# Optimization experiments

Hardware: AMD Instinct MI355X
Metric: run time of the kernel (lower is better)

The kernel has to match this reference:

```python
import jax, jax.numpy as jnp
import numpy as np

B, L, N, T, D, V, C = 128, 512, 1023, 511, 256, 50000, 511
EPS = 1e-6


def circular_correlation(a, b):
    # c_k = sum_i a_i * b_{(i+k) mod d}  == irfft(conj(rfft(a)) * rfft(b))
    d = a.shape[-1]
    c = jnp.fft.irfft(jnp.conj(jnp.fft.rfft(a, axis=-1)) * jnp.fft.rfft(b, axis=-1), n=d, axis=-1)
    return c / (jnp.linalg.norm(c, axis=-1, keepdims=True) + EPS)


def setup_inputs() -> dict:
    key = jax.random.key(0)
    k1, k2, k3, k4, k5, k6, k7, k8 = jax.random.split(key, 8)
    num_node = jnp.full((B,), N, dtype=jnp.int64 if jax.config.jax_enable_x64 else jnp.int32)
    # leaf slot index: leaves occupy node slots 0..L-1 (deterministic, no scatter collisions)
    slot = jnp.broadcast_to(jnp.arange(L, dtype=jnp.int32)[None, :], (B, L))
    vocab_id = jax.random.randint(k1, (B, L), 0, V, dtype=jnp.int32)
    leaf_content_id = jnp.stack([slot, vocab_id], axis=-1)  # [B, L, 2]
    content_mask = (jax.random.uniform(k2, (B, L)) < 0.9).astype(jnp.int32)
    ctype = jax.random.randint(k3, (B, T), 0, 3, dtype=jnp.int32)          # 0 = no-op, 1, 2 children
    parent = jax.random.randint(k4, (B, T), L, N, dtype=jnp.int32)         # internal node slots
    lchild = jax.random.randint(k5, (B, T), 0, N, dtype=jnp.int32)
    rchild = jax.random.randint(k6, (B, T), 0, N, dtype=jnp.int32)
    composition_info = jnp.stack([ctype, parent, lchild, rchild], axis=-1)  # [B, T, 4]
    emb_weight = jax.random.normal(k7, (V, D), dtype=jnp.float32) * 0.1
    lin_weight = jax.random.normal(k8, (C, D), dtype=jnp.float32) * 0.05
    lin_bias = jnp.zeros((C,), dtype=jnp.float32)
    return {"num_node": num_node, "leaf_content_id": leaf_content_id,
            "content_mask": content_mask, "composition_info": composition_info,
            "emb_weight": emb_weight, "lin_weight": lin_weight, "lin_bias": lin_bias}


def embed_leaf_nodes(leaf_content_id, content_mask, emb_weight):
    leaf_vec = emb_weight[leaf_content_id[:, :, 1]]          # [B, L, D]
    node_idx = leaf_content_id[:, :, 0]                      # [B, L]
    mask = content_mask != 0
    safe_idx = jnp.where(mask, node_idx, N)                  # N is out-of-bounds -> dropped
    vec = jnp.zeros((B, N, D), dtype=leaf_vec.dtype)
    vec = vec.at[jnp.arange(B)[:, None], safe_idx].set(leaf_vec, mode="drop")
    norm = jnp.linalg.norm(vec, axis=2, keepdims=True) + EPS
    return vec / norm


def compose(vec, composition_info):
    bidx = jnp.arange(B)

    def step(v, info):  # info: [B, 4] for one tree level
        t, p, l, r = info[:, 0], info[:, 1], info[:, 2], info[:, 3]
        safe_p = jnp.where(t > 0, p, 0)
        lv = v[bidx, l]                                      # [B, D]
        rv = v[bidx, r]
        two = circular_correlation(lv, rv)
        cur = v[bidx, safe_p]
        val = jnp.where((t == 1)[:, None], lv,
                        jnp.where((t == 2)[:, None], two, cur))
        return v.at[bidx, safe_p].set(val), None

    vec, _ = jax.lax.scan(step, vec, jnp.swapaxes(composition_info, 0, 1))
    return vec


def reference(num_node, leaf_content_id, content_mask, composition_info,
              emb_weight, lin_weight, lin_bias):
    vec = embed_leaf_nodes(leaf_content_id, content_mask, emb_weight)
    vec = compose(vec, composition_info)
    out = jnp.einsum("bnd,cd->bnc", vec, lin_weight) + lin_bias
    return out
```

## Files before the change

kernel.cpp:

```cpp
#include <hip/hip_runtime.h>

#define NB 128
#define NL 512
#define NN 1023
#define NT 511
#define ND 256
#define NC 511
#define EPSF 1e-6f

#define SRC_ZERO (-1)
#define SLOTC 4096
#define STEPC 8192

typedef __attribute__((ext_vector_type(8))) short short8;
typedef __attribute__((ext_vector_type(4))) float f32x4;
typedef __attribute__((ext_vector_type(2))) float f32x2;

__device__ __forceinline__ unsigned short f2bf(float f) {
  unsigned u = __builtin_bit_cast(unsigned, f);
  u += 0x7FFFu + ((u >> 16) & 1u);
  return (unsigned short)(u >> 16);
}

__global__ void __launch_bounds__(256) embed_scatter(
    const int* __restrict__ lcid, const int* __restrict__ cmask,
    const float* __restrict__ emb, const float* __restrict__ lw,
    float* __restrict__ leafbuf, unsigned short* __restrict__ vecb,
    unsigned short* __restrict__ wb) {
  if (blockIdx.x >= 16384) {
    int i   = (blockIdx.x - 16384) * 256 + threadIdx.x;
    int row = i >> 5;
    uint4 r = {0u, 0u, 0u, 0u};
    if (row < NC) {
      const float4* v4 = (const float4*)lw;
      float4 x = v4[2 * i], y = v4[2 * i + 1];
      r.x = (unsigned)f2bf(x.x) | ((unsigned)f2bf(x.y) << 16);
      r.y = (unsigned)f2bf(x.z) | ((unsigned)f2bf(x.w) << 16);
      r.z = (unsigned)f2bf(y.x) | ((unsigned)f2bf(y.y) << 16);
      r.w = (unsigned)f2bf(y.z) | ((unsigned)f2bf(y.w) << 16);
    }
    ((uint4*)wb)[i] = r;
    return;
  }
  int rid  = blockIdx.x * 4 + (threadIdx.x >> 6);
  int lane = threadIdx.x & 63;
  int slot = lcid[2 * rid];
  int vid  = lcid[2 * rid + 1];
  int msk  = cmask[rid];
  int b    = rid >> 9;
  float4 v = {0.f, 0.f, 0.f, 0.f};
  if (msk) v = ((const float4*)(emb + (size_t)vid * ND))[lane];
  float ss = v.x * v.x + v.y * v.y + v.z * v.z + v.w * v.w;
#pragma unroll
  for (int off = 32; off > 0; off >>= 1) ss += __shfl_down(ss, off, 64);
  ss = __shfl(ss, 0, 64);
  float inv = 1.0f / (sqrtf(ss) + EPSF);
  float4 o;
  o.x = v.x * inv; o.y = v.y * inv; o.z = v.z * inv; o.w = v.w * inv;
  ((float4*)(leafbuf + ((size_t)b * 512 + slot) * ND))[lane] = o;
  uint2 pk;
  pk.x = (unsigned)f2bf(o.x) | ((unsigned)f2bf(o.y) << 16);
  pk.y = (unsigned)f2bf(o.z) | ((unsigned)f2bf(o.w) << 16);
  ((uint2*)(vecb + ((size_t)b * NN + slot) * ND))[lane] = pk;
}

struct ComposeSh {
  int4 sinfo4[NT];
  int ptr_[NT];
  int lsA[NT], rsA[NT];
  int lvl[NT], fsrc[NT];
  int schedS[NT], schedL[NT], schedR[NT];
  int offs[512], cnt[512], cnt2[512];
  unsigned char deadF[NT], liveF[NT], lzero[512];
  float a_st[16][256];
  float b_st[16][512];
  float s_st[16][512];
  int changed, smax;
};
struct LeafGemmSh { short As[256 * 64]; short Ws[128 * 64]; };
union FuseSh { ComposeSh c; LeafGemmSh g; };

__global__ void __launch_bounds__(1024) compose_leafgemm(
    const int* __restrict__ info, const int* __restrict__ lcid,
    const int* __restrict__ cmask, const float* __restrict__ leafbuf,
    float* __restrict__ outbuf, int* __restrict__ fsrcG,
    const short* __restrict__ vecbS, const short* __restrict__ wbs,
    const float* __restrict__ bias, float* __restrict__ out) {
  __shared__ FuseSh sh;
  const int tid  = threadIdx.x;
  const int lane = tid & 63;
  const int wav  = tid >> 6;

  if (blockIdx.x < NB) {
    const int b = blockIdx.x;
    int4 (&sinfo4)[NT] = sh.c.sinfo4;
    int (&ptr_)[NT] = sh.c.ptr_;
    int (&lsA)[NT] = sh.c.lsA;  int (&rsA)[NT] = sh.c.rsA;
    int (&lvl)[NT] = sh.c.lvl;  int (&fsrc)[NT] = sh.c.fsrc;
    int (&schedS)[NT] = sh.c.schedS; int (&schedL)[NT] = sh.c.schedL;
    int (&schedR)[NT] = sh.c.schedR;
    int (&offs)[512] = sh.c.offs; int (&cnt)[512] = sh.c.cnt;
    int (&cnt2)[512] = sh.c.cnt2;
    unsigned char (&deadF)[NT] = sh.c.deadF;
    unsigned char (&liveF)[NT] = sh.c.liveF;
    unsigned char (&lzero)[512] = sh.c.lzero;
    float (&a_st)[16][256] = sh.c.a_st;
    float (&b_st)[16][512] = sh.c.b_st;
    float (&s_st)[16][512] = sh.c.s_st;
    int &changed = sh.c.changed; int &smax = sh.c.smax;

    const float* lb = leafbuf + (size_t)b * 512 * ND;
    float*       ob = outbuf + (size_t)b * NT * ND;

    const int4* ib4 = (const int4*)(info + (size_t)b * NT * 4);
    for (int i = tid; i < NT; i += 1024) sinfo4[i] = ib4[i];
    if (tid < 512) lzero[tid] = 1;
    if (tid == 0) smax = 0;
    __syncthreads();
    if (tid < NL) {
      int row = lcid[((size_t)b * NL + tid) * 2];
      lzero[row] = (cmask[(size_t)b * NL + tid] == 0) ? 1 : 0;
    }
    __syncthreads();

    const int t = tid;
    int4 m1 = {0, 0, 0, 0};
    if (t < NT) m1 = sinfo4[t];
    int l1 = -1, r1 = -1, f1 = -1;
    const int prow = 512 + t;
    for (int tp = 0; tp < NT; ++tp) {
      int4 wi = sinfo4[tp];
      if (wi.x > 0) {
        if (t < NT && tp < t) { if (wi.y == m1.z) l1 = tp; if (wi.y == m1.w) r1 = tp; }
        if (wi.y == prow) f1 = tp;
      }
    }
    __syncthreads();

    if (t < NT) {
      int v;
      if (m1.x == 2) v = SLOTC + t;
      else if (m1.x == 1) {
        if (m1.z < 512) v = m1.z;
        else v = (l1 >= 0) ? (STEPC + l1) : SRC_ZERO;
      } else v = SRC_ZERO;
      ptr_[t] = v;
    }
    __syncthreads();
    for (int it = 0; it < 10; ++it) {
      int v = 0;
      if (t < NT) { v = ptr_[t]; if (v >= STEPC) v = ptr_[v - STEPC]; }
      __syncthreads();
      if (t < NT) ptr_[t] = v;
      __syncthreads();
    }

    auto normv = [&](int v) -> int {
      if (v >= 0 && v < 512 && lzero[v]) return SRC_ZERO;
      return v;
    };
    auto collapseW = [&](int wstep) -> int {
      int v = (sinfo4[wstep].x == 2) ? (SLOTC + wstep) : ptr_[wstep];
      return normv(v);
    };
    if (t < NT) {
      if (m1.x == 2) {
        int a = (m1.z < 512) ? normv(m1.z) : ((l1 >= 0) ? collapseW(l1) : SRC_ZERO);
        int c = (m1.w < 512) ? normv(m1.w) : ((r1 >= 0) ? collapseW(r1) : SRC_ZERO);
        lsA[t] = a; rsA[t] = c;
        deadF[t] = (a == SRC_ZERO || c == SRC_ZERO) ? 1 : 0;
      } else {
        deadF[t] = 0;
      }
      liveF[t] = 0;
      fsrc[t] = (f1 >= 0) ? collapseW(f1) : SRC_ZERO;
    }
    __syncthreads();

    for (int rounds = 0; rounds < NT; ++rounds) {
      if (tid == 0) changed = 0;
      __syncthreads();
      if (t < NT && m1.x == 2 && !deadF[t]) {
        int a = lsA[t], c = rsA[t];
        if (a >= SLOTC && deadF[a - SLOTC]) { a = SRC_ZERO; lsA[t] = a; }
        if (c >= SLOTC && deadF[c - SLOTC]) { c = SRC_ZERO; rsA[t] = c; }
        if (a == SRC_ZERO || c == SRC_ZERO) { deadF[t] = 1; changed = 1; }
      }
      __syncthreads();
      if (!changed) break;
      __syncthreads();
    }

    if (t < NT) {
      int f = fsrc[t];
      if (f >= SLOTC && deadF[f - SLOTC]) { f = SRC_ZERO; fsrc[t] = f; }
      if (f >= SLOTC) liveF[f - SLOTC] = 1;
    }
    __syncthreads();
    for (int rounds = 0; rounds < NT; ++rounds) {
      if (tid == 0) changed = 0;
      __syncthreads();
      if (t < NT && m1.x == 2 && liveF[t] && !deadF[t]) {
        int a = lsA[t], c = rsA[t];
        if (a >= SLOTC && !liveF[a - SLOTC]) { liveF[a - SLOTC] = 1; changed = 1; }
        if (c >= SLOTC && !liveF[c - SLOTC]) { liveF[c - SLOTC] = 1; changed = 1; }
      }
      __syncthreads();
      if (!changed) break;
      __syncthreads();
    }

    const bool isLive = (t < NT && m1.x == 2 && liveF[t] && !deadF[t]);

    if (t < NT) lvl[t] = 0;
    __syncthreads();
    for (int rounds = 0; rounds < NT; ++rounds) {
      if (tid == 0) changed = 0;
      __syncthreads();
      if (isLive) {
        int nl = 1, a = lsA[t], c = rsA[t];
        if (a >= SLOTC) { int dl = lvl[a - SLOTC] + 1; if (dl > nl) nl = dl; }
        if (c >= SLOTC) { int dl = lvl[c - SLOTC] + 1; if (dl > nl) nl = dl; }
        if (nl > lvl[t]) { lvl[t] = nl; changed = 1; }
      }
      __syncthreads();
      if (!changed) break;
      __syncthreads();
    }
    if (isLive) atomicMax(&smax, lvl[t]);

    if (tid < 512) { cnt[tid] = 0; cnt2[tid] = 0; }
    __syncthreads();
    if (isLive) atomicAdd(&cnt[lvl[t]], 1);
    __syncthreads();
    if (tid < 512) offs[tid] = cnt[tid];
    __syncthreads();
    for (int k = 1; k < 512; k <<= 1) {
      int v = 0;
      if (tid < 512) { v = offs[tid]; if (tid >= k) v += offs[tid - k]; }
      __syncthreads();
      if (tid < 512) offs[tid] = v;
      __syncthreads();
    }
    if (isLive) {
      int d = lvl[t];
      int pos = offs[d - 1] + atomicAdd(&cnt2[d], 1);
      schedS[pos] = t; schedL[pos] = lsA[t]; schedR[pos] = rsA[t];
    }
    __syncthreads();

    const int maxd = smax;
    for (int d = 1; d <= maxd; ++d) {
      const int base = offs[d - 1];
      const int nops = cnt[d];
      const int nch  = (nops + 15) >> 4;
      for (int ch = 0; ch < nch; ++ch) {
        int rel = ch * 16 + wav;
        if (rel < nops) {
          int my = base + rel;
          int tt = schedS[my], ls = schedL[my], rs = schedR[my];
          const float* pa = (ls < 512) ? lb + (size_t)ls * ND
                                       : ob + (size_t)(ls - SLOTC) * ND;
          const float* pb = (rs < 512) ? lb + (size_t)rs * ND
                                       : ob + (size_t)(rs - SLOTC) * ND;
          float4 av = ((const float4*)pa)[lane];
          float4 bv = ((const float4*)pb)[lane];
          float nx = __shfl(bv.x, (lane + 1) & 63, 64);
          float4 sv = {bv.y, bv.z, bv.w, nx};
          ((float4*)a_st[wav])[lane]      = av;
          ((float4*)b_st[wav])[lane]      = bv;
          ((float4*)b_st[wav])[lane + 64] = bv;
          ((float4*)s_st[wav])[lane]      = sv;
          ((float4*)s_st[wav])[lane + 64] = sv;
          const float4* a4 = (const float4*)a_st[wav];
          const float4* b4 = (const float4*)b_st[wav];
          const float4* s4 = (const float4*)s_st[wav];
          f32x2 q0 = {0.f, 0.f}, q1 = {0.f, 0.f}, q2 = {0.f, 0.f}, q3 = {0.f, 0.f};
          float4 B0 = b4[lane];
          float4 S0 = s4[lane];
#pragma unroll 8
          for (int i = 0; i < 64; ++i) {
            float4 A  = a4[i];
            float4 B1 = b4[lane + i + 1];
            float4 S1 = s4[lane + i + 1];
            f32x2 Axy = {A.x, A.y},  Azw = {A.z, A.w};
            f32x2 Bxy = {B0.x, B0.y}, Bzw = {B0.z, B0.w};
            f32x2 Sxy = {S0.x, S0.y}, Szw = {S0.z, S0.w};
            f32x2 B1xy = {B1.x, B1.y}, S1xy = {S1.x, S1.y};
            q0 += Axy * Bxy;  q0 += Azw * Bzw;
            q1 += Axy * Sxy;  q1 += Azw * Szw;
            q2 += Axy * Bzw;  q2 += Azw * B1xy;
            q3 += Axy * Szw;  q3 += Azw * S1xy;
            B0 = B1; S0 = S1;
          }
          float c0 = q0.x + q0.y, c1 = q1.x + q1.y;
          float c2 = q2.x + q2.y, c3 = q3.x + q3.y;
          float ss = c0 * c0 + c1 * c1 + c2 * c2 + c3 * c3;
#pragma unroll
          for (int off = 32; off > 0; off >>= 1) ss += __shfl_down(ss, off, 64);
          ss = __shfl(ss, 0, 64);
          float inv = 1.f / (sqrtf(ss) + EPSF);
          float4 res;
          res.x = c0 * inv; res.y = c1 * inv; res.z = c2 * inv; res.w = c3 * inv;
          ((float4*)(ob + (size_t)tt * ND))[lane] = res;
        }
      }
      __syncthreads();
    }

    for (int i = tid; i < NT; i += 1024) fsrcG[b * NT + i] = fsrc[i];
    return;
  }

  const int gidx = blockIdx.x - NB;
  const int b  = gidx >> 3;
  const int mt = (gidx >> 2) & 1;
  const int ct = gidx & 3;
  const short* A = vecbS + ((size_t)b * NN + mt * 256) * ND;
  const int c0   = ct * 128;
  const int wr   = wav >> 1;
  const int wc   = wav & 1;
  const int frow = lane & 15;
  const int quad = lane >> 4;
  f32x4 acc[2][4];
#pragma unroll
  for (int i = 0; i < 2; ++i)
#pragma unroll
    for (int j = 0; j < 4; ++j) acc[i][j] = (f32x4){0.f, 0.f, 0.f, 0.f};

  for (int k0 = 0; k0 < ND; k0 += 64) {
#pragma unroll
    for (int i = 0; i < 2; ++i) {
      int idx = i * 1024 + tid;
      int row = idx >> 3;
      int chn = idx & 7;
      const short* ga = A + (size_t)row * ND + k0 + chn * 8;
      __builtin_amdgcn_global_load_lds(
          (const __attribute__((address_space(1))) void*)ga,
          (__attribute__((address_space(3))) void*)(sh.g.As + idx * 8), 16, 0, 0);
    }
    {
      int row = tid >> 3;
      int chn = tid & 7;
      const short* gw = wbs + (size_t)(c0 + row) * ND + k0 + chn * 8;
      __builtin_amdgcn_global_load_lds(
          (const __attribute__((address_space(1))) void*)gw,
          (__attribute__((address_space(3))) void*)(sh.g.Ws + tid * 8), 16, 0, 0);
    }
    __syncthreads();
#pragma unroll
    for (int ks = 0; ks < 2; ++ks) {
      short8 af[2], wf[4];
#pragma unroll
      for (int mi = 0; mi < 2; ++mi)
        af[mi] = *(const short8*)(sh.g.As + (wr * 32 + mi * 16 + frow) * 64 + ks * 32 + quad * 8);
#pragma unroll
      for (int ci = 0; ci < 4; ++ci)
        wf[ci] = *(const short8*)(sh.g.Ws + (wc * 64 + ci * 16 + frow) * 64 + ks * 32 + quad * 8);
#pragma unroll
      for (int mi = 0; mi < 2; ++mi)
#pragma unroll
        for (int ci = 0; ci < 4; ++ci)
          acc[mi][ci] = __builtin_amdgcn_mfma_f32_16x16x32_bf16(
              af[mi], wf[ci], acc[mi][ci], 0, 0, 0);
    }
    __syncthreads();
  }
#pragma unroll
  for (int mi = 0; mi < 2; ++mi) {
#pragma unroll
    for (int ci = 0; ci < 4; ++ci) {
      int col = c0 + wc * 64 + ci * 16 + frow;
      if (col < NC) {
        float bv = bias[col];
#pragma unroll
        for (int r = 0; r < 4; ++r) {
          int n = mt * 256 + wr * 32 + mi * 16 + quad * 4 + r;
          out[((size_t)b * NN + n) * NC + col] = acc[mi][ci][r] + bv;
        }
      }
    }
  }
}

__global__ void __launch_bounds__(256) gather_rows(
    const int* __restrict__ fsrcG, const float* __restrict__ leafbuf,
    const float* __restrict__ outbuf, unsigned short* __restrict__ vecb) {
  int rid  = blockIdx.x * 4 + (threadIdx.x >> 6);
  int lane = threadIdx.x & 63;
  int b    = rid / NT;
  int idx  = rid - b * NT;
  int s    = fsrcG[rid];
  float4 v = {0.f, 0.f, 0.f, 0.f};
  if (s >= 0) {
    const float* src = (s < 512)
        ? (leafbuf + ((size_t)b * 512 + s) * ND)
        : (outbuf + ((size_t)b * NT + (s - SLOTC)) * ND);
    v = ((const float4*)src)[lane];
  }
  uint2 pk;
  pk.x = (unsigned)f2bf(v.x) | ((unsigned)f2bf(v.y) << 16);
  pk.y = (unsigned)f2bf(v.z) | ((unsigned)f2bf(v.w) << 16);
  ((uint2*)(vecb + ((size_t)b * NN + 512 + idx) * ND))[lane] = pk;
}

union GemmSh {
  struct { short As[128 * 64]; short Ws[128 * 64]; } s;
  float epi[4][16][65];
};

__global__ void __launch_bounds__(256) gemm_int(
    const short* __restrict__ A, const short* __restrict__ W,
    const float* __restrict__ bias, float* __restrict__ out) {
  __shared__ GemmSh sh;
  int i = blockIdx.x;
  int mtile = (i >> 5) * 8 + (i & 7);
  int c     = (i >> 3) & 3;
  int b     = mtile >> 2;
  int mt    = mtile & 3;
  size_t arow = (size_t)b * NN + 512 + mt * 128;
  int tid  = threadIdx.x;
  int lane = tid & 63;
  int w    = tid >> 6;
  int c0   = c * 128;
  int wm   = (w & 1) * 64;
  int wc   = (w >> 1) * 64;
  int frow = lane & 15;
  int quad = lane >> 4;
  f32x4 acc[4][4];
#pragma unroll
  for (int a = 0; a < 4; ++a)
#pragma unroll
    for (int j = 0; j < 4; ++j) acc[a][j] = (f32x4){0.f, 0.f, 0.f, 0.f};

  for (int k0 = 0; k0 < ND; k0 += 64) {
#pragma unroll
    for (int a = 0; a < 4; ++a) {
      int idx = a * 256 + tid;
      int row = idx >> 3;
      int ch  = idx & 7;
      int chs = ch ^ (row & 7);
      const short* ga = A + (arow + row) * ND + k0 + chs * 8;
      const short* gw = W + (size_t)(c0 + row) * ND + k0 + chs * 8;
      __builtin_amdgcn_global_load_lds(
          (const __attribute__((address_space(1))) void*)ga,
          (__attribute__((address_space(3))) void*)(sh.s.As + idx * 8), 16, 0, 0);
      __builtin_amdgcn_global_load_lds(
          (const __attribute__((address_space(1))) void*)gw,
          (__attribute__((address_space(3))) void*)(sh.s.Ws + idx * 8), 16, 0, 0);
    }
    __syncthreads();
#pragma unroll
    for (int ks = 0; ks < 2; ++ks) {
      short8 af[4], wf[4];
#pragma unroll
      for (int mi = 0; mi < 4; ++mi) {
        int r = wm + mi * 16 + frow;
        int cc = (ks * 4 + quad) ^ (r & 7);
        af[mi] = *(const short8*)(sh.s.As + r * 64 + cc * 8);
      }
#pragma unroll
      for (int ci = 0; ci < 4; ++ci) {
        int r = wc + ci * 16 + frow;
        int cc = (ks * 4 + quad) ^ (r & 7);
        wf[ci] = *(const short8*)(sh.s.Ws + r * 64 + cc * 8);
      }
#pragma unroll
      for (int mi = 0; mi < 4; ++mi)
#pragma unroll
        for (int ci = 0; ci < 4; ++ci)
          acc[mi][ci] = __builtin_amdgcn_mfma_f32_16x16x32_bf16(
              af[mi], wf[ci], acc[mi][ci], 0, 0, 0);
    }
    __syncthreads();
  }

  int colg = c0 + wc + lane;
  float bv = (colg < NC) ? bias[colg] : 0.f;
#pragma unroll
  for (int mi = 0; mi < 4; ++mi) {
#pragma unroll
    for (int ci = 0; ci < 4; ++ci)
#pragma unroll
      for (int r = 0; r < 4; ++r)
        sh.epi[w][quad * 4 + r][ci * 16 + frow] = acc[mi][ci][r];
    if (colg < NC) {
      int nbase = 512 + mt * 128 + wm + mi * 16;
#pragma unroll
      for (int rr = 0; rr < 16; ++rr) {
        int n = nbase + rr;
        if (n < NN)
          out[((size_t)b * NN + n) * NC + colg] = sh.epi[w][rr][lane] + bv;
      }
    }
  }
}

extern "C" void kernel_launch(void* const* d_in, const int* in_sizes, int n_in,
                              void* d_out, int out_size, void* d_ws, size_t ws_size,
                              hipStream_t stream) {
  const int*   lcid  = (const int*)d_in[1];
  const int*   cmask = (const int*)d_in[2];
  const int*   cinfo = (const int*)d_in[3];
  const float* emb   = (const float*)d_in[4];
  const float* lw    = (const float*)d_in[5];
  const float* lbias = (const float*)d_in[6];
  float*       out   = (float*)d_out;

  char* ws = (char*)d_ws;
  float*          leafbuf = (float*)ws;
  float*          outbuf  = (float*)(ws + 67108864);
  unsigned short* vecb    = (unsigned short*)(ws + 134086656);
  unsigned short* wb      = (unsigned short*)(ws + 201129984);
  int*            fsrcG   = (int*)d_out + (size_t)512 * NC;

  embed_scatter<<<16448, 256, 0, stream>>>(lcid, cmask, emb, lw,
                                           leafbuf, vecb, wb);
  compose_leafgemm<<<NB + 1024, 1024, 0, stream>>>(
      cinfo, lcid, cmask, leafbuf, outbuf, fsrcG,
      (const short*)vecb, (const short*)wb, lbias, out);
  gather_rows<<<NB * NT / 4, 256, 0, stream>>>(fsrcG, leafbuf, outbuf, vecb);
  gemm_int<<<2048, 256, 0, stream>>>(
      (const short*)vecb, (const short*)wb, lbias, out);
}
```

Baseline: 480.5 us.

## Fuse row gather into compose kernel via inverse-source lists, drop gather launch

The compose blocks now build a per-block inverse map (linked lists via atomicExch) from each computed correlation result to all internal node slots that take their final value from it. Each result is written directly as bf16 into the GEMM input buffer, and slots sourced from leaves or zero are filled up front. This removes the separate gather_rows kernel launch and its fp32 reread of outbuf. It also remaps the leaf-GEMM block indices so blocks sharing a column tile are grouped together. In exchange, the compose blocks do some extra serialized writes inside their critical path.

```diff
diff --git a/kernel.cpp b/kernel.cpp
--- a/kernel.cpp
+++ b/kernel.cpp
@@ -69,6 +69,7 @@
   int ptr_[NT];
   int lsA[NT], rsA[NT];
   int lvl[NT], fsrc[NT];
+  int invHead[NT], invNext[NT];
   int schedS[NT], schedL[NT], schedR[NT];
   int offs[512], cnt[512], cnt2[512];
   unsigned char deadF[NT], liveF[NT], lzero[512];
@@ -83,7 +84,7 @@
 __global__ void __launch_bounds__(1024) compose_leafgemm(
     const int* __restrict__ info, const int* __restrict__ lcid,
     const int* __restrict__ cmask, const float* __restrict__ leafbuf,
-    float* __restrict__ outbuf, int* __restrict__ fsrcG,
+    float* __restrict__ outbuf, unsigned short* __restrict__ vecbW,
     const short* __restrict__ vecbS, const short* __restrict__ wbs,
     const float* __restrict__ bias, float* __restrict__ out) {
   __shared__ FuseSh sh;
@@ -97,6 +98,7 @@
     int (&ptr_)[NT] = sh.c.ptr_;
     int (&lsA)[NT] = sh.c.lsA;  int (&rsA)[NT] = sh.c.rsA;
     int (&lvl)[NT] = sh.c.lvl;  int (&fsrc)[NT] = sh.c.fsrc;
+    int (&invHead)[NT] = sh.c.invHead; int (&invNext)[NT] = sh.c.invNext;
     int (&schedS)[NT] = sh.c.schedS; int (&schedL)[NT] = sh.c.schedL;
     int (&schedR)[NT] = sh.c.schedR;
     int (&offs)[512] = sh.c.offs; int (&cnt)[512] = sh.c.cnt;
@@ -111,6 +113,7 @@
 
     const float* lb = leafbuf + (size_t)b * 512 * ND;
     float*       ob = outbuf + (size_t)b * NT * ND;
+    unsigned short* vb = vecbW + ((size_t)b * NN + 512) * ND;
 
     const int4* ib4 = (const int4*)(info + (size_t)b * NT * 4);
     for (int i = tid; i < NT; i += 1024) sinfo4[i] = ib4[i];
@@ -209,6 +212,23 @@
       if (!changed) break;
       __syncthreads();
     }
+
+    if (t < NT) invHead[t] = -1;
+    __syncthreads();
+    if (t < NT && fsrc[t] >= SLOTC)
+      invNext[t] = atomicExch(&invHead[fsrc[t] - SLOTC], t);
+    for (int i = wav; i < NT; i += 16) {
+      int s = fsrc[i];
+      if (s < SLOTC) {
+        float4 v = {0.f, 0.f, 0.f, 0.f};
+        if (s >= 0) v = ((const float4*)(lb + (size_t)s * ND))[lane];
+        uint2 pk;
+        pk.x = (unsigned)f2bf(v.x) | ((unsigned)f2bf(v.y) << 16);
+        pk.y = (unsigned)f2bf(v.z) | ((unsigned)f2bf(v.w) << 16);
+        ((uint2*)(vb + (size_t)i * ND))[lane] = pk;
+      }
+    }
+    __syncthreads();
 
     const bool isLive = (t < NT && m1.x == 2 && liveF[t] && !deadF[t]);
 
@@ -303,19 +323,28 @@
           float4 res;
           res.x = c0 * inv; res.y = c1 * inv; res.z = c2 * inv; res.w = c3 * inv;
           ((float4*)(ob + (size_t)tt * ND))[lane] = res;
+          int idx = invHead[tt];
+          if (idx >= 0) {
+            uint2 pk;
+            pk.x = (unsigned)f2bf(res.x) | ((unsigned)f2bf(res.y) << 16);
+            pk.y = (unsigned)f2bf(res.z) | ((unsigned)f2bf(res.w) << 16);
+            do {
+              ((uint2*)(vb + (size_t)idx * ND))[lane] = pk;
+              idx = invNext[idx];
+            } while (idx >= 0);
+          }
         }
       }
       __syncthreads();
     }
-
-    for (int i = tid; i < NT; i += 1024) fsrcG[b * NT + i] = fsrc[i];
     return;
   }
 
   const int gidx = blockIdx.x - NB;
-  const int b  = gidx >> 3;
-  const int mt = (gidx >> 2) & 1;
-  const int ct = gidx & 3;
+  const int pair = (gidx >> 5) * 8 + (gidx & 7);
+  const int ct   = (gidx >> 3) & 3;
+  const int b  = pair >> 1;
+  const int mt = pair & 1;
   const short* A = vecbS + ((size_t)b * NN + mt * 256) * ND;
   const int c0   = ct * 128;
   const int wr   = wav >> 1;
@@ -381,27 +410,6 @@
       }
     }
   }
-}
-
-__global__ void __launch_bounds__(256) gather_rows(
-    const int* __restrict__ fsrcG, const float* __restrict__ leafbuf,
-    const float* __restrict__ outbuf, unsigned short* __restrict__ vecb) {
-  int rid  = blockIdx.x * 4 + (threadIdx.x >> 6);
-  int lane = threadIdx.x & 63;
-  int b    = rid / NT;
-  int idx  = rid - b * NT;
-  int s    = fsrcG[rid];
-  float4 v = {0.f, 0.f, 0.f, 0.f};
-  if (s >= 0) {
-    const float* src = (s < 512)
-        ? (leafbuf + ((size_t)b * 512 + s) * ND)
-        : (outbuf + ((size_t)b * NT + (s - SLOTC)) * ND);
-    v = ((const float4*)src)[lane];
-  }
-  uint2 pk;
-  pk.x = (unsigned)f2bf(v.x) | ((unsigned)f2bf(v.y) << 16);
-  pk.y = (unsigned)f2bf(v.z) | ((unsigned)f2bf(v.w) << 16);
-  ((uint2*)(vecb + ((size_t)b * NN + 512 + idx) * ND))[lane] = pk;
 }
 
 union GemmSh {
@@ -512,14 +520,12 @@
   float*          outbuf  = (float*)(ws + 67108864);
   unsigned short* vecb    = (unsigned short*)(ws + 134086656);
   unsigned short* wb      = (unsigned short*)(ws + 201129984);
-  int*            fsrcG   = (int*)d_out + (size_t)512 * NC;
 
   embed_scatter<<<16448, 256, 0, stream>>>(lcid, cmask, emb, lw,
                                            leafbuf, vecb, wb);
   compose_leafgemm<<<NB + 1024, 1024, 0, stream>>>(
-      cinfo, lcid, cmask, leafbuf, outbuf, fsrcG,
+      cinfo, lcid, cmask, leafbuf, outbuf, vecb,
       (const short*)vecb, (const short*)wb, lbias, out);
-  gather_rows<<<NB * NT / 4, 256, 0, stream>>>(fsrcG, leafbuf, outbuf, vecb);
   gemm_int<<<2048, 256, 0, stream>>>(
       (const short*)vecb, (const short*)wb, lbias, out);
 }
```

Result: slower. 523.1 us (+8.9%).
